# Kernel tuning notes

Measured on AMD Instinct MI355X. Metric: run time of the kernel, lower is better.

## Reference

```python
import jax, jax.numpy as jnp
import numpy as np

B, D, N, DM, V = 1024, 256, 256, 128, 512  # batch, dsym, nrole/max_len, dmorphosyn, affix vocab


def setup_inputs() -> dict:
    key = jax.random.key(0)
    ks = jax.random.split(key, 8)
    return {
        "stem_form": jax.random.normal(ks[0], (B, D, N), jnp.float32),
        "morphosyn": jax.random.normal(ks[1], (B, DM), jnp.float32),
        "pivot_logits": jax.random.normal(ks[2], (2, 2, B, 5, N), jnp.float32),
        "W_affix": jax.random.normal(ks[3], (DM, V), jnp.float32) / np.sqrt(DM).astype(np.float32),
        "affix_vocab": jax.random.normal(ks[4], (V, D, N), jnp.float32),
        "alpha": jax.random.normal(ks[5], (2,), jnp.float32),
        "beta": jax.random.normal(ks[6], (2,), jnp.float32),
        "phi": jax.random.normal(ks[7], (5,), jnp.float32),
        "max_len": N,
    }


def reference(stem_form, morphosyn, pivot_logits, W_affix, affix_vocab, alpha, beta, phi, max_len):
    # mixture weights over 2 directions x 2 locations x 5 features
    a = jax.nn.softmax(alpha, -1)   # [2]
    b = jax.nn.softmax(beta, -1)    # [2]
    f = jax.nn.softmax(phi, -1)     # [5]
    # AffixVocab: morphosyntactic attention over affix vocabulary -> affix form
    attn = jax.nn.softmax(morphosyn @ W_affix, -1)            # [B, V]
    affix_form = jnp.einsum('bv,vdn->bdn', attn, affix_vocab)  # [B, D, N]
    # pivoter: soft one-hot pivot distributions over positions
    pivots = jax.nn.softmax(pivot_logits, -1)                  # [2, 2, B, 5, N]
    C = jnp.cumsum(pivots, -1)                                 # cumulative pivot mass
    # fused triple loop: sum_{drn,loc,ftr} alpha*beta*phi * morph_op(stem, affix, pivot)
    # morph_op = soft splice: keep stem before pivot, write affix after pivot.
    # Since morph_op is affine in C, the weighted sum collapses onto a single mask.
    wC = jnp.einsum('i,j,k,ijbkn->bn', a, b, f, C)[:, None, :]  # [B, 1, N]
    out_form = stem_form * (1.0 - wC) + affix_form * wC          # [B, D, N]
    return out_form
```

## Files before the change

### kernel.cpp

```cpp
#include <hip/hip_runtime.h>
#include <hip/hip_bf16.h>
#include <stdint.h>

typedef __bf16 bf16x8 __attribute__((ext_vector_type(8)));
typedef float f32x4 __attribute__((ext_vector_type(4)));

static __device__ __forceinline__ unsigned short f2bf(float x) {
    union { float f; unsigned u; } v; v.f = x;
    unsigned r = v.u + 0x7FFFu + ((v.u >> 16) & 1u);
    return (unsigned short)(r >> 16);
}

static __device__ __forceinline__ void gload_lds16(const void* g, void* l) {
    auto gp = (const unsigned int __attribute__((address_space(1)))*)(reinterpret_cast<uintptr_t>(g));
    auto lp = (unsigned int __attribute__((address_space(3)))*)(reinterpret_cast<uintptr_t>(l));
    __builtin_amdgcn_global_load_lds(gp, lp, 16, 0, 0);
}

__global__ void attn_kernel(const float* __restrict__ morphosyn,
                            const float* __restrict__ W,
                            unsigned short* __restrict__ attn_sw) {
    const int b = blockIdx.x;
    const int t = threadIdx.x;
    __shared__ float ms[128];
    __shared__ float red[4];
    if (t < 128) ms[t] = morphosyn[b * 128 + t];
    __syncthreads();
    float acc0 = 0.f, acc1 = 0.f;
    #pragma unroll 8
    for (int dm = 0; dm < 128; ++dm) {
        float m = ms[dm];
        acc0 = fmaf(m, W[dm * 512 + t], acc0);
        acc1 = fmaf(m, W[dm * 512 + t + 256], acc1);
    }
    const int lane = t & 63, wid = t >> 6;
    float mx = fmaxf(acc0, acc1);
    #pragma unroll
    for (int o = 32; o; o >>= 1) mx = fmaxf(mx, __shfl_xor(mx, o));
    if (lane == 0) red[wid] = mx;
    __syncthreads();
    mx = fmaxf(fmaxf(red[0], red[1]), fmaxf(red[2], red[3]));
    __syncthreads();
    float e0 = __expf(acc0 - mx), e1 = __expf(acc1 - mx);
    float sm = e0 + e1;
    #pragma unroll
    for (int o = 32; o; o >>= 1) sm += __shfl_xor(sm, o);
    if (lane == 0) red[wid] = sm;
    __syncthreads();
    sm = red[0] + red[1] + red[2] + red[3];
    const float inv = 1.0f / sm;
    const int swz = (b >> 2) & 3;
    #pragma unroll
    for (int h = 0; h < 2; ++h) {
        int v = t + h * 256;
        int ae = (v >> 5) * 32 + ((((v >> 3) & 3) ^ swz) << 3) + (v & 7);
        attn_sw[b * 512 + ae] = f2bf((h ? e1 : e0) * inv);
    }
}

__global__ void wc_kernel(const float* __restrict__ logits,
                          const float* __restrict__ alpha,
                          const float* __restrict__ beta,
                          const float* __restrict__ phi,
                          float* __restrict__ wC) {
    const int b = blockIdx.x;
    const int t = threadIdx.x;
    const int lane = t & 63, wid = t >> 6;
    __shared__ float part[4][256];
    __shared__ float wsum[4];

    float a0 = alpha[0], a1 = alpha[1];
    float am = fmaxf(a0, a1);
    float ea0 = __expf(a0 - am), ea1 = __expf(a1 - am);
    float as = ea0 + ea1;
    float b0 = beta[0], b1 = beta[1];
    float bm = fmaxf(b0, b1);
    float eb0 = __expf(b0 - bm), eb1 = __expf(b1 - bm);
    float bs = eb0 + eb1;
    float p[5];
    float pm = -1e30f;
    #pragma unroll
    for (int k = 0; k < 5; ++k) { p[k] = phi[k]; pm = fmaxf(pm, p[k]); }
    float ps = 0.f;
    #pragma unroll
    for (int k = 0; k < 5; ++k) { p[k] = __expf(p[k] - pm); ps += p[k]; }
    const float wa[2] = {ea0 / as, ea1 / as}, wb[2] = {eb0 / bs, eb1 / bs};

    f32x4 accv = {0.f, 0.f, 0.f, 0.f};
    #pragma unroll
    for (int s5 = 0; s5 < 5; ++s5) {
        int sl = wid * 5 + s5;
        int i = sl >= 10;
        int j = (sl / 5) & 1;
        int k = sl - (sl / 5) * 5;
        const float* base = logits + ((size_t)(((i * 2 + j) * 1024 + b) * 5 + k)) * 256;
        f32x4 x = *(const f32x4*)(base + lane * 4);
        float mx = fmaxf(fmaxf(x[0], x[1]), fmaxf(x[2], x[3]));
        #pragma unroll
        for (int o = 32; o; o >>= 1) mx = fmaxf(mx, __shfl_xor(mx, o));
        f32x4 e;
        float sm = 0.f;
        #pragma unroll
        for (int r = 0; r < 4; ++r) { e[r] = __expf(x[r] - mx); sm += e[r]; }
        #pragma unroll
        for (int o = 32; o; o >>= 1) sm += __shfl_xor(sm, o);
        float w = wa[i] * wb[j] * (p[k] / ps) / sm;
        #pragma unroll
        for (int r = 0; r < 4; ++r) accv[r] += w * e[r];
    }
    *(f32x4*)&part[wid][lane * 4] = accv;
    __syncthreads();
    float v = part[0][t] + part[1][t] + part[2][t] + part[3][t];
    #pragma unroll
    for (int o = 1; o < 64; o <<= 1) {
        float u = __shfl_up(v, o);
        if (lane >= o) v += u;
    }
    if (lane == 63) wsum[wid] = v;
    __syncthreads();
    float offv = 0.f;
    for (int w2 = 0; w2 < wid; ++w2) offv += wsum[w2];
    wC[b * 256 + t] = v + offv;
}

__global__ void conv_kernel(const float* __restrict__ vocab, unsigned short* __restrict__ Bt) {
    const int n0 = blockIdx.x * 16;
    const int t = threadIdx.x;
    __shared__ unsigned int T[16 * 256];
    #pragma unroll
    for (int it = 0; it < 4; ++it) {
        int p = it * 256 + t;
        int v = (p >> 2) * 2;
        int col4 = p & 3;
        const float* g0 = vocab + (size_t)v * 65536 + n0 + col4 * 4;
        float4 a = *(const float4*)g0;
        float4 c = *(const float4*)(g0 + 65536);
        #pragma unroll
        for (int j = 0; j < 4; ++j) {
            int n = col4 * 4 + j;
            unsigned d = (unsigned)f2bf((&a.x)[j]) | ((unsigned)f2bf((&c.x)[j]) << 16);
            T[n * 256 + (v >> 1)] = d;
        }
    }
    __syncthreads();
    #pragma unroll
    for (int it = 0; it < 4; ++it) {
        int qq = it * 256 + t;
        int r = qq >> 6, c = qq & 63;
        int swz = ((n0 + r) >> 2) & 3;
        int dc = (c & ~3) | ((c & 3) ^ swz);
        uint4 d = *(const uint4*)(&T[r * 256 + c * 4]);
        *(uint4*)(Bt + (size_t)(n0 + r) * 512 + dc * 8) = d;
    }
}

__global__ __launch_bounds__(512, 4) void gemm_kernel(
        const unsigned short* __restrict__ attn_sw,
        const unsigned short* __restrict__ Bt,
        const float* __restrict__ stem,
        const float* __restrict__ wC,
        float* __restrict__ out) {
    const int bid = blockIdx.x;
    const int xcd = bid & 7, s = bid >> 3;
    const int m0 = (s & 7) << 7;
    const int n0 = ((xcd << 5) + (s >> 3)) << 8;
    const int t = threadIdx.x;
    const int lane = t & 63, wid = t >> 6;
    const int wr = wid >> 2, wcn = wid & 3;
    const int q = lane >> 4, rl = lane & 15;
    const int soff = ((q ^ ((rl >> 2) & 3)) << 4);

    __shared__ __align__(16) unsigned short ldsb[24576];

    f32x4 acc[4][4];
    const f32x4 z = {0.f, 0.f, 0.f, 0.f};
    #pragma unroll
    for (int i = 0; i < 4; ++i)
        #pragma unroll
        for (int j = 0; j < 4; ++j) acc[i][j] = z;

    const unsigned short* a_src = attn_sw + (size_t)(m0 + (t >> 2)) * 512 + (t & 3) * 8;
    const unsigned short* b_src = Bt + (size_t)(n0 + (t >> 2)) * 512 + (t & 3) * 8;

#define STAGE(kt) do { \
    unsigned short* dst_ = ldsb + (((kt) & 1) ? 12288 : 0); \
    const int ko_ = (kt) * 32; \
    gload_lds16(a_src + ko_, dst_ + t * 8); \
    _Pragma("unroll") \
    for (int i_ = 0; i_ < 2; ++i_) \
        gload_lds16(b_src + (size_t)i_ * 65536 + ko_, dst_ + 4096 + (i_ * 512 + t) * 8); \
} while (0)

#define KSTEP(kt, STG, VMSTR) do { \
    if (STG) STAGE((kt) + 1); \
    asm volatile("s_waitcnt vmcnt(" VMSTR ")" ::: "memory"); \
    __builtin_amdgcn_s_barrier(); \
    __builtin_amdgcn_sched_barrier(0); \
    const char* abase_ = (const char*)(ldsb + (((kt) & 1) ? 12288 : 0)); \
    const char* bbase_ = abase_ + 8192; \
    bf16x8 af_[4], bfv_[4]; \
    _Pragma("unroll") \
    for (int f_ = 0; f_ < 4; ++f_) \
        af_[f_] = *(const bf16x8*)(abase_ + (wr * 64 + f_ * 16 + rl) * 64 + soff); \
    _Pragma("unroll") \
    for (int j_ = 0; j_ < 4; ++j_) \
        bfv_[j_] = *(const bf16x8*)(bbase_ + (wcn * 64 + j_ * 16 + rl) * 64 + soff); \
    __builtin_amdgcn_s_setprio(1); \
    _Pragma("unroll") \
    for (int fm_ = 0; fm_ < 4; ++fm_) \
        _Pragma("unroll") \
        for (int j_ = 0; j_ < 4; ++j_) \
            acc[fm_][j_] = __builtin_amdgcn_mfma_f32_16x16x32_bf16( \
                af_[fm_], bfv_[j_], acc[fm_][j_], 0, 0, 0); \
    __builtin_amdgcn_s_setprio(0); \
    __builtin_amdgcn_sched_barrier(0); \
    __builtin_amdgcn_s_barrier(); \
} while (0)

    STAGE(0);
    KSTEP(0, 1, "3");  KSTEP(1, 1, "3");  KSTEP(2, 1, "3");  KSTEP(3, 1, "3");
    KSTEP(4, 1, "3");  KSTEP(5, 1, "3");  KSTEP(6, 1, "3");  KSTEP(7, 1, "3");
    KSTEP(8, 1, "3");  KSTEP(9, 1, "3");  KSTEP(10, 1, "3"); KSTEP(11, 1, "3");
    KSTEP(12, 1, "3"); KSTEP(13, 1, "3"); KSTEP(14, 1, "3"); KSTEP(15, 0, "0");
#undef STAGE
#undef KSTEP
    __syncthreads();

    float* cs = (float*)ldsb;
    #pragma unroll
    for (int sb = 0; sb < 4; ++sb) {
        if (sb) __syncthreads();
        if (wr == (sb >> 1)) {
            #pragma unroll
            for (int fh = 0; fh < 2; ++fh) {
                int fm = (sb & 1) * 2 + fh;
                #pragma unroll
                for (int n = 0; n < 4; ++n) {
                    int c = wcn * 64 + n * 16 + rl;
                    #pragma unroll
                    for (int i = 0; i < 4; ++i)
                        cs[(fh * 16 + q * 4 + i) * 260 + c] = acc[fm][n][i];
                }
            }
        }
        __syncthreads();
        #pragma unroll
        for (int r = 0; r < 4; ++r) {
            int row = wid * 4 + r;
            int b = m0 + sb * 32 + row;
            size_t gb = (size_t)b * 65536 + (size_t)n0 + lane * 4;
            f32x4 cv = *(const f32x4*)&cs[row * 260 + lane * 4];
            f32x4 sv = *(const f32x4*)&stem[gb];
            f32x4 wv = *(const f32x4*)&wC[((size_t)b << 8) + lane * 4];
            f32x4 ov;
            #pragma unroll
            for (int jj = 0; jj < 4; ++jj)
                ov[jj] = sv[jj] + (cv[jj] - sv[jj]) * wv[jj];
            *(f32x4*)&out[gb] = ov;
        }
    }
}

__global__ void gemm_fb(const unsigned short* __restrict__ attn_sw,
                        const float* __restrict__ vocab,
                        const float* __restrict__ stem,
                        const float* __restrict__ wC,
                        float* __restrict__ out) {
    const int tile_m = blockIdx.x & 7;
    const int tile_n = blockIdx.x >> 3;
    const int m0 = tile_m << 7;
    const int n0 = tile_n << 7;
    const int t = threadIdx.x;
    const int lane = t & 63;
    const int wv = t >> 6;
    const int wm = wv >> 1, wn = wv & 1;

    __shared__ unsigned short Asl[128 * 32];
    __shared__ unsigned short Bsl[128 * 32];

    f32x4 acc[4][4];
    const f32x4 z = {0.f, 0.f, 0.f, 0.f};
    #pragma unroll
    for (int i = 0; i < 4; ++i)
        #pragma unroll
        for (int j = 0; j < 4; ++j) acc[i][j] = z;

    const unsigned short* a_base = attn_sw + ((size_t)m0 << 9);
    const int q = lane >> 4;
    const int rl = lane & 15;

    for (int ks = 0; ks < 16; ++ks) {
        #pragma unroll
        for (int it = 0; it < 2; ++it) {
            int idx = it * 256 + t;
            int r = idx >> 2, blk = idx & 3;
            gload_lds16(a_base + r * 512 + ks * 32 + blk * 8, Asl + idx * 8);
        }
        #pragma unroll
        for (int it = 0; it < 2; ++it) {
            int lin = it * 256 + t;
            int pair = lin >> 5;
            int chunk = lin & 31;
            int k = pair * 2;
            const float* g0 = vocab + (size_t)(ks * 32 + k) * 65536 + n0 + chunk * 4;
            float4 v0 = *(const float4*)g0;
            float4 v1 = *(const float4*)(g0 + 65536);
            #pragma unroll
            for (int j = 0; j < 4; ++j) {
                int n = chunk * 4 + j;
                unsigned d = (unsigned)f2bf((&v0.x)[j]) | ((unsigned)f2bf((&v1.x)[j]) << 16);
                int ae = n * 32 + ((((k >> 3) ^ ((n >> 2) & 3))) << 3) + (k & 7);
                *(unsigned*)((char*)Bsl + ae * 2) = d;
            }
        }
        __syncthreads();
        bf16x8 af[4], bfr[4];
        #pragma unroll
        for (int f = 0; f < 4; ++f) {
            int r = wm * 64 + f * 16 + rl;
            af[f] = *(const bf16x8*)((const char*)Asl + r * 64 + ((q ^ ((r >> 2) & 3)) << 4));
            int c = wn * 64 + f * 16 + rl;
            bfr[f] = *(const bf16x8*)((const char*)Bsl + c * 64 + ((q ^ ((c >> 2) & 3)) << 4));
        }
        __syncthreads();
        #pragma unroll
        for (int fm = 0; fm < 4; ++fm)
            #pragma unroll
            for (int fn = 0; fn < 4; ++fn)
                acc[fm][fn] = __builtin_amdgcn_mfma_f32_16x16x32_bf16(af[fm], bfr[fn], acc[fm][fn], 0, 0, 0);
    }

    #pragma unroll
    for (int fm = 0; fm < 4; ++fm) {
        int rbase = m0 + wm * 64 + fm * 16 + ((lane >> 4) << 2);
        #pragma unroll
        for (int fn = 0; fn < 4; ++fn) {
            int c = n0 + wn * 64 + fn * 16 + (lane & 15);
            #pragma unroll
            for (int i = 0; i < 4; ++i) {
                int b = rbase + i;
                float w = wC[(b << 8) + (c & 255)];
                size_t o = ((size_t)b << 16) + (size_t)c;
                float sv = stem[o];
                out[o] = sv + (acc[fm][fn][i] - sv) * w;
            }
        }
    }
}

extern "C" void kernel_launch(void* const* d_in, const int* in_sizes, int n_in,
                              void* d_out, int out_size, void* d_ws, size_t ws_size,
                              hipStream_t stream) {
    const float* stem    = (const float*)d_in[0];
    const float* morpho  = (const float*)d_in[1];
    const float* logits  = (const float*)d_in[2];
    const float* W       = (const float*)d_in[3];
    const float* vocab   = (const float*)d_in[4];
    const float* alpha   = (const float*)d_in[5];
    const float* beta    = (const float*)d_in[6];
    const float* phi     = (const float*)d_in[7];
    float* out = (float*)d_out;

    unsigned short* attn_sw = (unsigned short*)d_ws;
    float* wC = (float*)((char*)d_ws + (1 << 20));
    unsigned short* Bt = (unsigned short*)((char*)d_ws + (2 << 20));

    const size_t need = (size_t)(2 << 20) + (size_t)64 * 1024 * 1024;

    attn_kernel<<<1024, 256, 0, stream>>>(morpho, W, attn_sw);
    wc_kernel<<<1024, 256, 0, stream>>>(logits, alpha, beta, phi, wC);
    if (ws_size >= need) {
        conv_kernel<<<4096, 256, 0, stream>>>(vocab, Bt);
        gemm_kernel<<<2048, 512, 0, stream>>>(attn_sw, Bt, stem, wC, out);
    } else {
        gemm_fb<<<4096, 256, 0, stream>>>(attn_sw, vocab, stem, wC, out);
    }
}
```

Measured before the change: 249.2 us.

## Switch GEMM tile to 256x128 and use triple-buffered LDS with prefetch distance two

The tile shape changes from 128(M)x256(N) to 256(M)x128(N), with the warp grid reorganized to 4x2. The LDS staging goes from double to triple buffering, so each step prefetches two k-steps ahead, and the trailing barrier per k-step is dropped. The epilogue is rewritten for the new tile shape. The aim is to hide global-load latency and cut synchronization, at the cost of more LDS (72 KB), which may reduce occupancy.

After: 247.5 us. Within noise of the previous version (-0.7%).

```diff
diff --git a/kernel.cpp b/kernel.cpp
--- a/kernel.cpp
+++ b/kernel.cpp
@@ -162,15 +162,15 @@
         float* __restrict__ out) {
     const int bid = blockIdx.x;
     const int xcd = bid & 7, s = bid >> 3;
-    const int m0 = (s & 7) << 7;
-    const int n0 = ((xcd << 5) + (s >> 3)) << 8;
+    const int m0 = (s & 3) << 8;
+    const int n0 = ((xcd << 6) + (s >> 2)) << 7;
     const int t = threadIdx.x;
     const int lane = t & 63, wid = t >> 6;
-    const int wr = wid >> 2, wcn = wid & 3;
+    const int wr = wid >> 1, wcn = wid & 1;
     const int q = lane >> 4, rl = lane & 15;
     const int soff = ((q ^ ((rl >> 2) & 3)) << 4);
 
-    __shared__ __align__(16) unsigned short ldsb[24576];
+    __shared__ __align__(16) unsigned short ldsb[36864];
 
     f32x4 acc[4][4];
     const f32x4 z = {0.f, 0.f, 0.f, 0.f};
@@ -183,21 +183,20 @@
     const unsigned short* b_src = Bt + (size_t)(n0 + (t >> 2)) * 512 + (t & 3) * 8;
 
 #define STAGE(kt) do { \
-    unsigned short* dst_ = ldsb + (((kt) & 1) ? 12288 : 0); \
+    unsigned short* dst_ = ldsb + ((kt) % 3) * 12288; \
     const int ko_ = (kt) * 32; \
     gload_lds16(a_src + ko_, dst_ + t * 8); \
-    _Pragma("unroll") \
-    for (int i_ = 0; i_ < 2; ++i_) \
-        gload_lds16(b_src + (size_t)i_ * 65536 + ko_, dst_ + 4096 + (i_ * 512 + t) * 8); \
+    gload_lds16(a_src + 65536 + ko_, dst_ + 4096 + t * 8); \
+    gload_lds16(b_src + ko_, dst_ + 8192 + t * 8); \
 } while (0)
 
 #define KSTEP(kt, STG, VMSTR) do { \
-    if (STG) STAGE((kt) + 1); \
     asm volatile("s_waitcnt vmcnt(" VMSTR ")" ::: "memory"); \
     __builtin_amdgcn_s_barrier(); \
     __builtin_amdgcn_sched_barrier(0); \
-    const char* abase_ = (const char*)(ldsb + (((kt) & 1) ? 12288 : 0)); \
-    const char* bbase_ = abase_ + 8192; \
+    if (STG) STAGE((kt) + 2); \
+    const char* abase_ = (const char*)(ldsb + ((kt) % 3) * 12288); \
+    const char* bbase_ = abase_ + 16384; \
     bf16x8 af_[4], bfv_[4]; \
     _Pragma("unroll") \
     for (int f_ = 0; f_ < 4; ++f_) \
@@ -214,14 +213,13 @@
                 af_[fm_], bfv_[j_], acc[fm_][j_], 0, 0, 0); \
     __builtin_amdgcn_s_setprio(0); \
     __builtin_amdgcn_sched_barrier(0); \
-    __builtin_amdgcn_s_barrier(); \
 } while (0)
 
-    STAGE(0);
+    STAGE(0); STAGE(1);
     KSTEP(0, 1, "3");  KSTEP(1, 1, "3");  KSTEP(2, 1, "3");  KSTEP(3, 1, "3");
     KSTEP(4, 1, "3");  KSTEP(5, 1, "3");  KSTEP(6, 1, "3");  KSTEP(7, 1, "3");
     KSTEP(8, 1, "3");  KSTEP(9, 1, "3");  KSTEP(10, 1, "3"); KSTEP(11, 1, "3");
-    KSTEP(12, 1, "3"); KSTEP(13, 1, "3"); KSTEP(14, 1, "3"); KSTEP(15, 0, "0");
+    KSTEP(12, 1, "3"); KSTEP(13, 1, "3"); KSTEP(14, 0, "3"); KSTEP(15, 0, "0");
 #undef STAGE
 #undef KSTEP
     __syncthreads();
@@ -230,28 +228,28 @@
     #pragma unroll
     for (int sb = 0; sb < 4; ++sb) {
         if (sb) __syncthreads();
-        if (wr == (sb >> 1)) {
-            #pragma unroll
-            for (int fh = 0; fh < 2; ++fh) {
-                int fm = (sb & 1) * 2 + fh;
+        if (wr == sb) {
+            #pragma unroll
+            for (int fm = 0; fm < 4; ++fm) {
                 #pragma unroll
                 for (int n = 0; n < 4; ++n) {
                     int c = wcn * 64 + n * 16 + rl;
                     #pragma unroll
                     for (int i = 0; i < 4; ++i)
-                        cs[(fh * 16 + q * 4 + i) * 260 + c] = acc[fm][n][i];
+                        cs[(fm * 16 + q * 4 + i) * 132 + c] = acc[fm][n][i];
                 }
             }
         }
         __syncthreads();
         #pragma unroll
-        for (int r = 0; r < 4; ++r) {
-            int row = wid * 4 + r;
-            int b = m0 + sb * 32 + row;
-            size_t gb = (size_t)b * 65536 + (size_t)n0 + lane * 4;
-            f32x4 cv = *(const f32x4*)&cs[row * 260 + lane * 4];
+        for (int i2 = 0; i2 < 4; ++i2) {
+            int row = i2 * 16 + (t >> 5);
+            int col = (t & 31) * 4;
+            int b = m0 + sb * 64 + row;
+            size_t gb = (size_t)b * 65536 + (size_t)n0 + col;
+            f32x4 cv = *(const f32x4*)&cs[row * 132 + col];
             f32x4 sv = *(const f32x4*)&stem[gb];
-            f32x4 wv = *(const f32x4*)&wC[((size_t)b << 8) + lane * 4];
+            f32x4 wv = *(const f32x4*)&wC[((size_t)b << 8) + (n0 & 255) + col];
             f32x4 ov;
             #pragma unroll
             for (int jj = 0; jj < 4; ++jj)
```
